# Optimization experiments

Measured on AMD Instinct MI355X. Metric: run time of the kernel, lower is better.

## Reference

```python
import jax, jax.numpy as jnp
import numpy as np

D_MODEL = 1024
H = 16
D_K = D_MODEL // H
NEG = -1e9


def setup_inputs() -> dict:
    key = jax.random.key(0)
    ks = jax.random.split(key, 13)
    B, S = 4, 2048
    q = jax.random.normal(ks[0], (B, S, D_MODEL), dtype=jnp.float32)
    k = jax.random.normal(ks[1], (B, S, D_MODEL), dtype=jnp.float32)
    v = jax.random.normal(ks[2], (B, S, D_MODEL), dtype=jnp.float32)
    mask = jax.random.randint(ks[3], (B, 1, S, S), 0, 2, dtype=jnp.int32)
    s = 1.0 / np.sqrt(D_MODEL)
    wq = jax.random.uniform(ks[4], (D_MODEL, D_MODEL), jnp.float32, -s, s)
    bq = jax.random.uniform(ks[5], (D_MODEL,), jnp.float32, -s, s)
    wk = jax.random.uniform(ks[6], (D_MODEL, D_MODEL), jnp.float32, -s, s)
    bk = jax.random.uniform(ks[7], (D_MODEL,), jnp.float32, -s, s)
    wv = jax.random.uniform(ks[8], (D_MODEL, D_MODEL), jnp.float32, -s, s)
    bv = jax.random.uniform(ks[9], (D_MODEL,), jnp.float32, -s, s)
    wo = jax.random.uniform(ks[10], (D_MODEL, D_MODEL), jnp.float32, -s, s)
    bo = jax.random.uniform(ks[11], (D_MODEL,), jnp.float32, -s, s)
    return {"q": q, "k": k, "v": v, "mask": mask,
            "wq": wq, "bq": bq, "wk": wk, "bk": bk,
            "wv": wv, "bv": bv, "wo": wo, "bo": bo}


def reference(q, k, v, mask, wq, bq, wk, bk, wv, bv, wo, bo):
    B, S, _ = q.shape
    # projections (torch Linear: x @ W.T + b)
    query = q @ wq.T + bq
    key_ = k @ wk.T + bk
    value = v @ wv.T + bv
    # [B, S, H, D_K] -> [B, H, S, D_K]
    query = query.reshape(B, S, H, D_K).transpose(0, 2, 1, 3)
    key_ = key_.reshape(B, S, H, D_K).transpose(0, 2, 1, 3)
    value = value.reshape(B, S, H, D_K).transpose(0, 2, 1, 3)
    scores = jnp.einsum('bhqd,bhkd->bhqk', query, key_) / jnp.sqrt(jnp.float32(D_K))
    scores = jnp.where(mask == 0, jnp.float32(NEG), scores)
    attn = jax.nn.softmax(scores, axis=-1)  # dropout p=0 -> identity
    x = jnp.einsum('bhqk,bhkd->bhqd', attn, value)
    x = x.transpose(0, 2, 1, 3).reshape(B, S, D_MODEL)
    return x @ wo.T + bo
```

## Files before the change

kernel.cpp:

```cpp
#include <hip/hip_runtime.h>
#include <stdint.h>
#include <stddef.h>


typedef unsigned short ushort_t;
typedef unsigned long long u64;
typedef __attribute__((ext_vector_type(8))) short short8;
typedef __attribute__((ext_vector_type(4))) float floatx4;
typedef __attribute__((ext_vector_type(4))) unsigned short ushort4v;
typedef __attribute__((ext_vector_type(4))) unsigned int uint4v;

#define QSCALE (0.125f * 1.4426950408889634f)

__device__ __forceinline__ ushort_t f2bf(float f) {
    union { float ff; unsigned int i; } v; v.ff = f;
    unsigned int u = v.i;
    return (ushort_t)((u + 0x7fffu + ((u >> 16) & 1u)) >> 16);
}
__device__ __forceinline__ unsigned int pk2(float a, float b) {
    unsigned int r;
    asm("v_cvt_pk_bf16_f32 %0, %1, %2" : "=v"(r) : "v"(a), "v"(b));
    return r;
}
__device__ __forceinline__ float fexp2(float x) {
#if __has_builtin(__builtin_amdgcn_exp2f)
    return __builtin_amdgcn_exp2f(x);
#else
    return exp2f(x);
#endif
}
__device__ __forceinline__ void g2l16(const void* g, void* l) {
    __builtin_amdgcn_global_load_lds(
        (const __attribute__((address_space(1))) void*)(uintptr_t)g,
        (__attribute__((address_space(3))) void*)(uint32_t)(uintptr_t)l,
        16, 0, 0);
}

__global__ __launch_bounds__(256) void conv_w4(
    const float* __restrict__ w0, const float* __restrict__ w1,
    const float* __restrict__ w2, const float* __restrict__ w3,
    ushort_t* __restrict__ out)
{
    const int seg = blockIdx.y;
    const float* src = (seg == 0) ? w0 : (seg == 1) ? w1 : (seg == 2) ? w2 : w3;
    const int i = blockIdx.x * 256 + threadIdx.x;
    const float4 v = ((const float4*)src)[i];
    ushort4v o;
    o.x = f2bf(v.x); o.y = f2bf(v.y); o.z = f2bf(v.z); o.w = f2bf(v.w);
    ((ushort4v*)(out + (size_t)seg * 1024 * 1024))[i] = o;
}

__global__ __launch_bounds__(256) void mask_pack(
    const int* __restrict__ m, u64* __restrict__ out)
{
    const int gid = blockIdx.x * 256 + threadIdx.x;
    const u64 bits = __ballot(m[gid] != 0);
    if ((threadIdx.x & 63) == 0) out[gid >> 6] = bits;
}

template <int AF32>
__device__ __forceinline__ void gemm_core(
    const void* __restrict__ Ain, const ushort_t* __restrict__ W,
    const float* __restrict__ bias, void* __restrict__ Cout,
    float scale, int mode)
{
    constexpr int N = 1024, K = 1024;
    __shared__ alignas(16) ushort_t As[2][128 * 32];
    __shared__ alignas(16) ushort_t Bs[2][128 * 32];

    const int tid  = threadIdx.x;
    const int lane = tid & 63;
    const int w    = tid >> 6;
    const int quad = lane >> 4;
    const int l16  = lane & 15;
    const int wm = w >> 1, wn = w & 1;
    const int bm = blockIdx.x * 128, bn = blockIdx.y * 128;

    const int ar0 = tid >> 2,         acs0 = ((tid & 3) ^ (ar0 & 3)) * 8;
    const int ar1 = (tid + 256) >> 2, acs1 = ((tid & 3) ^ (ar1 & 3)) * 8;

    const ushort_t* Wst0 = W + (size_t)(bn + ar0) * K + acs0;
    const ushort_t* Wst1 = W + (size_t)(bn + ar1) * K + acs1;

    const int arow = tid >> 1, ahalf = tid & 1;
    const float* Af = (const float*)Ain + (size_t)(bm + arow) * K + ahalf * 16;
    const int ac0 = ((2 * ahalf + 0) ^ (arow & 3)) * 8;
    const int ac1 = ((2 * ahalf + 1) ^ (arow & 3)) * 8;

    const ushort_t* Ast0 = (const ushort_t*)Ain + (size_t)(bm + ar0) * K + acs0;
    const ushort_t* Ast1 = (const ushort_t*)Ain + (size_t)(bm + ar1) * K + acs1;

    const int ksw = (quad ^ (l16 & 3)) * 8;
    int asoff[4], bsoff[4];
#pragma unroll
    for (int i = 0; i < 4; i++) {
        asoff[i] = (wm * 64 + i * 16 + l16) * 32 + ksw;
        bsoff[i] = (wn * 64 + i * 16 + l16) * 32 + ksw;
    }

    floatx4 acc[4][4] = {};

    if (AF32) {
        const float4* ap = (const float4*)Af;
        const float4 f0 = ap[0], f1 = ap[1], f2 = ap[2], f3 = ap[3];
        uint4v c0, c1;
        c0.x = pk2(f0.x, f0.y); c0.y = pk2(f0.z, f0.w);
        c0.z = pk2(f1.x, f1.y); c0.w = pk2(f1.z, f1.w);
        c1.x = pk2(f2.x, f2.y); c1.y = pk2(f2.z, f2.w);
        c1.z = pk2(f3.x, f3.y); c1.w = pk2(f3.z, f3.w);
        *(uint4v*)&As[0][arow * 32 + ac0] = c0;
        *(uint4v*)&As[0][arow * 32 + ac1] = c1;
    } else {
        g2l16(Ast0, &As[0][tid * 8]);
        g2l16(Ast1, &As[0][(tid + 256) * 8]);
    }
    g2l16(Wst0, &Bs[0][tid * 8]);
    g2l16(Wst1, &Bs[0][(tid + 256) * 8]);
    __syncthreads();

    int cur = 0;
    for (int kt = 0; kt < K; kt += 32) {
        const int nxt = kt + 32;
        float4 f0, f1, f2, f3;
        if (nxt < K) {
            if (AF32) {
                const float4* ap = (const float4*)(Af + nxt);
                f0 = ap[0]; f1 = ap[1]; f2 = ap[2]; f3 = ap[3];
            } else {
                g2l16(Ast0 + nxt, &As[cur ^ 1][tid * 8]);
                g2l16(Ast1 + nxt, &As[cur ^ 1][(tid + 256) * 8]);
            }
            g2l16(Wst0 + nxt, &Bs[cur ^ 1][tid * 8]);
            g2l16(Wst1 + nxt, &Bs[cur ^ 1][(tid + 256) * 8]);
        }

        short8 af[4], bf[4];
#pragma unroll
        for (int i = 0; i < 4; i++) af[i] = *(const short8*)&As[cur][asoff[i]];
#pragma unroll
        for (int i = 0; i < 4; i++) bf[i] = *(const short8*)&Bs[cur][bsoff[i]];
#pragma unroll
        for (int mi = 0; mi < 4; mi++)
#pragma unroll
            for (int ni = 0; ni < 4; ni++)
                acc[mi][ni] = __builtin_amdgcn_mfma_f32_16x16x32_bf16(
                    af[mi], bf[ni], acc[mi][ni], 0, 0, 0);

        if (AF32 && nxt < K) {
            uint4v c0, c1;
            c0.x = pk2(f0.x, f0.y); c0.y = pk2(f0.z, f0.w);
            c0.z = pk2(f1.x, f1.y); c0.w = pk2(f1.z, f1.w);
            c1.x = pk2(f2.x, f2.y); c1.y = pk2(f2.z, f2.w);
            c1.z = pk2(f3.x, f3.y); c1.w = pk2(f3.z, f3.w);
            *(uint4v*)&As[cur ^ 1][arow * 32 + ac0] = c0;
            *(uint4v*)&As[cur ^ 1][arow * 32 + ac1] = c1;
        }
        __syncthreads();
        cur ^= 1;
    }

#pragma unroll
    for (int ni = 0; ni < 4; ni++) {
        const int n = bn + wn * 64 + ni * 16 + l16;
        const float bv_ = bias[n];
#pragma unroll
        for (int mi = 0; mi < 4; mi++) {
            const int mbase = bm + wm * 64 + mi * 16 + quad * 4;
            if (mode == 2) {
                const int b_ = mbase >> 11, s0 = mbase & 2047;
                const int h = n >> 6, d = n & 63;
                ushort4v pk_;
#pragma unroll
                for (int r = 0; r < 4; r++)
                    pk_[r] = f2bf((acc[mi][ni][r] + bv_) * scale);
                *(ushort4v*)&((ushort_t*)Cout)[
                    (((size_t)(b_ * 16 + h)) * 64 + d) * 2048 + s0] = pk_;
            } else {
#pragma unroll
                for (int r = 0; r < 4; r++) {
                    const int m = mbase + r;
                    const float of = (acc[mi][ni][r] + bv_) * scale;
                    if (mode == 0) {
                        ((float*)Cout)[(size_t)m * N + n] = of;
                    } else {
                        const int b_ = m >> 11, s = m & 2047;
                        const int h = n >> 6, d = n & 63;
                        ((ushort_t*)Cout)[(((size_t)(b_ * 16 + h)) * 2048 + s) * 64 + d]
                            = f2bf(of);
                    }
                }
            }
        }
    }
}

__global__ __launch_bounds__(256, 2) void gemm_qkv(
    const float* __restrict__ q, const float* __restrict__ k,
    const float* __restrict__ v, const ushort_t* __restrict__ Wb,
    const float* __restrict__ bq, const float* __restrict__ bk,
    const float* __restrict__ bv,
    ushort_t* __restrict__ Qp, ushort_t* __restrict__ Kp,
    ushort_t* __restrict__ Vtp)
{
    const int z = blockIdx.z;
    const float* A = (z == 0) ? q : (z == 1) ? k : v;
    const ushort_t* W = Wb + (size_t)z * 1024 * 1024;
    const float* bi = (z == 0) ? bq : (z == 1) ? bk : bv;
    void* C = (z == 0) ? (void*)Qp : (z == 1) ? (void*)Kp : (void*)Vtp;
    const float sc = (z == 0) ? QSCALE : 1.0f;
    const int mode = (z == 2) ? 2 : 1;
    gemm_core<1>(A, W, bi, C, sc, mode);
}

__global__ __launch_bounds__(256, 2) void gemm_out(
    const ushort_t* __restrict__ X, const ushort_t* __restrict__ W,
    const float* __restrict__ bo, float* __restrict__ out)
{
    gemm_core<0>(X, W, bo, out, 1.0f, 0);
}

__global__ __launch_bounds__(256, 4) void attn(
    const ushort_t* __restrict__ Q,
    const ushort_t* __restrict__ Kk,
    const ushort_t* __restrict__ Vt,
    const u64* __restrict__ mb,
    ushort_t* __restrict__ X)
{
    constexpr int S = 2048;
    __shared__ alignas(16) ushort_t Ks[2][64 * 64];
    __shared__ alignas(16) ushort_t Vs[2][64 * 64];
    __shared__ alignas(16) ushort_t Ps[4][16 * 64];

    const int tid  = threadIdx.x;
    const int lane = tid & 63;
    const int w    = tid >> 6;
    const int quad = lane >> 4;
    const int l16  = lane & 15;
    const int bh = blockIdx.x;
    const int b  = bh >> 4, h = bh & 15;
    const int qbase = blockIdx.y * 64 + w * 16;
    const int qlane = qbase + l16;

    const int r0 = tid >> 3,         cs0 = ((tid & 7) ^ (r0 & 7)) * 8;
    const int r1 = (tid + 256) >> 3, cs1 = ((tid & 7) ^ (r1 & 7)) * 8;

    const ushort_t* Kst0 = &Kk[((size_t)bh * S + r0) * 64 + cs0];
    const ushort_t* Kst1 = &Kk[((size_t)bh * S + r1) * 64 + cs1];
    const ushort_t* Vst0 = &Vt[((size_t)bh * 64 + r0) * S + cs0];
    const ushort_t* Vst1 = &Vt[((size_t)bh * 64 + r1) * S + cs1];

    const int swz = l16 & 7;
    int kvoff[2][4], pfoff[2], pwoff[4];
#pragma unroll
    for (int ks = 0; ks < 2; ks++) {
        pfoff[ks] = l16 * 64 + (((ks * 4 + quad) ^ swz) * 8);
#pragma unroll
        for (int ni = 0; ni < 4; ni++)
            kvoff[ks][ni] = (ni * 16 + l16) * 64 + (((ks * 4 + quad) ^ swz) * 8);
    }
#pragma unroll
    for (int ni = 0; ni < 4; ni++)
        pwoff[ni] = l16 * 64 + (((ni * 2 + (quad >> 1)) ^ swz) * 8) + (quad & 1) * 4;
    ushort_t* Psw = &Ps[w][0];

    short8 qf[2];
#pragma unroll
    for (int ks = 0; ks < 2; ks++)
        qf[ks] = *(const short8*)&Q[((size_t)bh * S + qlane) * 64 + ks * 32 + quad * 8];

    short8 onesv;
#pragma unroll
    for (int i = 0; i < 8; i++) onesv[i] = (short)0x3F80;

    const u64* mrow = mb + ((size_t)b * S + qlane) * 32;

    floatx4 o[4] = {};
    floatx4 lf = {};

    g2l16(Kst0, &Ks[0][tid * 8]);
    g2l16(Kst1, &Ks[0][(tid + 256) * 8]);
    g2l16(Vst0, &Vs[0][tid * 8]);
    g2l16(Vst1, &Vs[0][(tid + 256) * 8]);
    __syncthreads();

    int cur = 0;
    for (int kt = 0; kt < 32; kt++) {
        if (kt < 31) {
            g2l16(Kst0 + (kt + 1) * 4096, &Ks[cur ^ 1][tid * 8]);
            g2l16(Kst1 + (kt + 1) * 4096, &Ks[cur ^ 1][(tid + 256) * 8]);
            g2l16(Vst0 + (kt + 1) * 64,   &Vs[cur ^ 1][tid * 8]);
            g2l16(Vst1 + (kt + 1) * 64,   &Vs[cur ^ 1][(tid + 256) * 8]);
        }
        const ushort_t* Ksc = &Ks[cur][0];
        const ushort_t* Vsc = &Vs[cur][0];

        floatx4 s[4] = {};
#pragma unroll
        for (int ks = 0; ks < 2; ks++)
#pragma unroll
            for (int ni = 0; ni < 4; ni++)
                s[ni] = __builtin_amdgcn_mfma_f32_16x16x32_bf16(
                    *(const short8*)&Ksc[kvoff[ks][ni]], qf[ks], s[ni], 0, 0, 0);

        const u64 mw = mrow[kt];
#pragma unroll
        for (int ni = 0; ni < 4; ni++) {
            const unsigned int t = (unsigned int)(mw >> (ni * 16 + quad * 4));
#pragma unroll
            for (int r = 0; r < 4; r++)
                s[ni][r] = (t & (1u << r)) ? fexp2(s[ni][r]) : 0.f;
        }

#pragma unroll
        for (int ni = 0; ni < 4; ni++) {
            const unsigned int lo = pk2(s[ni][0], s[ni][1]);
            const unsigned int hi = pk2(s[ni][2], s[ni][3]);
            const unsigned long long dv = ((unsigned long long)hi << 32) | lo;
            *(unsigned long long*)&Psw[pwoff[ni]] = dv;
        }

#pragma unroll
        for (int ks = 0; ks < 2; ks++) {
            const short8 pf = *(const short8*)&Psw[pfoff[ks]];
            lf = __builtin_amdgcn_mfma_f32_16x16x32_bf16(onesv, pf, lf, 0, 0, 0);
#pragma unroll
            for (int ni = 0; ni < 4; ni++)
                o[ni] = __builtin_amdgcn_mfma_f32_16x16x32_bf16(
                    *(const short8*)&Vsc[kvoff[ks][ni]], pf, o[ni], 0, 0, 0);
        }
        __syncthreads();
        cur ^= 1;
    }

    const float inv = 1.0f / lf[0];
#pragma unroll
    for (int ni = 0; ni < 4; ni++) {
        ushort4v pk_;
#pragma unroll
        for (int r = 0; r < 4; r++) pk_[r] = f2bf(o[ni][r] * inv);
        *(ushort4v*)&X[((size_t)b * S + qlane) * 1024 + h * 64 + ni * 16 + quad * 4] = pk_;
    }
}

extern "C" void kernel_launch(void* const* d_in, const int* in_sizes, int n_in,
                              void* d_out, int out_size, void* d_ws, size_t ws_size,
                              hipStream_t stream) {
    const float* q    = (const float*)d_in[0];
    const float* k    = (const float*)d_in[1];
    const float* v    = (const float*)d_in[2];
    const int*   mask = (const int*)d_in[3];
    const float* wq   = (const float*)d_in[4];
    const float* bq   = (const float*)d_in[5];
    const float* wk   = (const float*)d_in[6];
    const float* bk   = (const float*)d_in[7];
    const float* wv   = (const float*)d_in[8];
    const float* bv   = (const float*)d_in[9];
    const float* wo   = (const float*)d_in[10];
    const float* bo   = (const float*)d_in[11];

    const size_t MB = 1024 * 1024;
    uint8_t* ws = (uint8_t*)d_ws;
    ushort_t* Wb   = (ushort_t*)(ws);
    u64*      mbits= (u64*)(ws + 8 * MB);
    ushort_t* Qp   = (ushort_t*)(ws + 10 * MB);
    ushort_t* Kp   = (ushort_t*)(ws + 26 * MB);
    ushort_t* Vtp  = (ushort_t*)(ws + 42 * MB);
    ushort_t* Xp   = (ushort_t*)(ws + 58 * MB);

    dim3 blk(256);
    const int gW = (1024 * 1024) / 1024;
    const int gM = (4 * 2048 * 2048) / 256;

    conv_w4<<<dim3(gW, 4), blk, 0, stream>>>(wq, wk, wv, wo, Wb);
    mask_pack<<<gM, blk, 0, stream>>>(mask, mbits);

    gemm_qkv<<<dim3(64, 8, 3), blk, 0, stream>>>(q, k, v, Wb, bq, bk, bv,
                                                 Qp, Kp, Vtp);

    attn<<<dim3(64, 32), blk, 0, stream>>>(Qp, Kp, Vtp, mbits, Xp);

    gemm_out<<<dim3(64, 8), blk, 0, stream>>>(Xp, Wb + 3 * MB, bo, (float*)d_out);
}
```

Before: 430.8 us.

## Pre-convert activations to bf16 and triple-buffer GEMM with async loads

Adds a separate kernel that converts the fp32 q/k/v activations to bf16 so the QKV GEMM can load its A tiles with direct global-to-LDS copies instead of register loads plus in-loop conversion. The GEMM main loop becomes a three-stage LDS ring with explicit vmcnt waits and a single barrier per k-step, keeping two tiles in flight. The launch-bounds occupancy hint rises from 2 to 3 blocks. The trade is an extra pass over the activations in memory (read fp32, write bf16) and more LDS per block. Xp and Qb share a workspace region, which is safe only because the QKV GEMM finishes before attention writes Xp.

After: 419.5 us. 1.03x faster.

```diff
diff --git a/kernel.cpp b/kernel.cpp
--- a/kernel.cpp
+++ b/kernel.cpp
@@ -50,6 +50,24 @@
     ((ushort4v*)(out + (size_t)seg * 1024 * 1024))[i] = o;
 }
 
+__global__ __launch_bounds__(256) void cvt_a(
+    const float* __restrict__ q, const float* __restrict__ k,
+    const float* __restrict__ v,
+    ushort_t* __restrict__ Qb, ushort_t* __restrict__ Kb,
+    ushort_t* __restrict__ Vb)
+{
+    const int z = blockIdx.y;
+    const float* src = (z == 0) ? q : (z == 1) ? k : v;
+    ushort_t* dst = (z == 0) ? Qb : (z == 1) ? Kb : Vb;
+    const int i = blockIdx.x * 256 + threadIdx.x;
+    const float4 f0 = ((const float4*)src)[i * 2];
+    const float4 f1 = ((const float4*)src)[i * 2 + 1];
+    uint4v c;
+    c.x = pk2(f0.x, f0.y); c.y = pk2(f0.z, f0.w);
+    c.z = pk2(f1.x, f1.y); c.w = pk2(f1.z, f1.w);
+    ((uint4v*)dst)[i] = c;
+}
+
 __global__ __launch_bounds__(256) void mask_pack(
     const int* __restrict__ m, u64* __restrict__ out)
 {
@@ -58,15 +76,14 @@
     if ((threadIdx.x & 63) == 0) out[gid >> 6] = bits;
 }
 
-template <int AF32>
 __device__ __forceinline__ void gemm_core(
-    const void* __restrict__ Ain, const ushort_t* __restrict__ W,
+    const ushort_t* __restrict__ Ain, const ushort_t* __restrict__ W,
     const float* __restrict__ bias, void* __restrict__ Cout,
     float scale, int mode)
 {
     constexpr int N = 1024, K = 1024;
-    __shared__ alignas(16) ushort_t As[2][128 * 32];
-    __shared__ alignas(16) ushort_t Bs[2][128 * 32];
+    __shared__ alignas(16) ushort_t As[3][128 * 32];
+    __shared__ alignas(16) ushort_t Bs[3][128 * 32];
 
     const int tid  = threadIdx.x;
     const int lane = tid & 63;
@@ -78,17 +95,10 @@
 
     const int ar0 = tid >> 2,         acs0 = ((tid & 3) ^ (ar0 & 3)) * 8;
     const int ar1 = (tid + 256) >> 2, acs1 = ((tid & 3) ^ (ar1 & 3)) * 8;
-
+    const ushort_t* Ast0 = Ain + (size_t)(bm + ar0) * K + acs0;
+    const ushort_t* Ast1 = Ain + (size_t)(bm + ar1) * K + acs1;
     const ushort_t* Wst0 = W + (size_t)(bn + ar0) * K + acs0;
     const ushort_t* Wst1 = W + (size_t)(bn + ar1) * K + acs1;
-
-    const int arow = tid >> 1, ahalf = tid & 1;
-    const float* Af = (const float*)Ain + (size_t)(bm + arow) * K + ahalf * 16;
-    const int ac0 = ((2 * ahalf + 0) ^ (arow & 3)) * 8;
-    const int ac1 = ((2 * ahalf + 1) ^ (arow & 3)) * 8;
-
-    const ushort_t* Ast0 = (const ushort_t*)Ain + (size_t)(bm + ar0) * K + acs0;
-    const ushort_t* Ast1 = (const ushort_t*)Ain + (size_t)(bm + ar1) * K + acs1;
 
     const int ksw = (quad ^ (l16 & 3)) * 8;
     int asoff[4], bsoff[4];
@@ -100,64 +110,51 @@
 
     floatx4 acc[4][4] = {};
 
-    if (AF32) {
-        const float4* ap = (const float4*)Af;
-        const float4 f0 = ap[0], f1 = ap[1], f2 = ap[2], f3 = ap[3];
-        uint4v c0, c1;
-        c0.x = pk2(f0.x, f0.y); c0.y = pk2(f0.z, f0.w);
-        c0.z = pk2(f1.x, f1.y); c0.w = pk2(f1.z, f1.w);
-        c1.x = pk2(f2.x, f2.y); c1.y = pk2(f2.z, f2.w);
-        c1.z = pk2(f3.x, f3.y); c1.w = pk2(f3.z, f3.w);
-        *(uint4v*)&As[0][arow * 32 + ac0] = c0;
-        *(uint4v*)&As[0][arow * 32 + ac1] = c1;
-    } else {
-        g2l16(Ast0, &As[0][tid * 8]);
-        g2l16(Ast1, &As[0][(tid + 256) * 8]);
-    }
-    g2l16(Wst0, &Bs[0][tid * 8]);
-    g2l16(Wst1, &Bs[0][(tid + 256) * 8]);
-    __syncthreads();
-
-    int cur = 0;
-    for (int kt = 0; kt < K; kt += 32) {
-        const int nxt = kt + 32;
-        float4 f0, f1, f2, f3;
-        if (nxt < K) {
-            if (AF32) {
-                const float4* ap = (const float4*)(Af + nxt);
-                f0 = ap[0]; f1 = ap[1]; f2 = ap[2]; f3 = ap[3];
-            } else {
-                g2l16(Ast0 + nxt, &As[cur ^ 1][tid * 8]);
-                g2l16(Ast1 + nxt, &As[cur ^ 1][(tid + 256) * 8]);
-            }
-            g2l16(Wst0 + nxt, &Bs[cur ^ 1][tid * 8]);
-            g2l16(Wst1 + nxt, &Bs[cur ^ 1][(tid + 256) * 8]);
-        }
-
-        short8 af[4], bf[4];
-#pragma unroll
-        for (int i = 0; i < 4; i++) af[i] = *(const short8*)&As[cur][asoff[i]];
-#pragma unroll
-        for (int i = 0; i < 4; i++) bf[i] = *(const short8*)&Bs[cur][bsoff[i]];
-#pragma unroll
-        for (int mi = 0; mi < 4; mi++)
-#pragma unroll
-            for (int ni = 0; ni < 4; ni++)
-                acc[mi][ni] = __builtin_amdgcn_mfma_f32_16x16x32_bf16(
-                    af[mi], bf[ni], acc[mi][ni], 0, 0, 0);
-
-        if (AF32 && nxt < K) {
-            uint4v c0, c1;
-            c0.x = pk2(f0.x, f0.y); c0.y = pk2(f0.z, f0.w);
-            c0.z = pk2(f1.x, f1.y); c0.w = pk2(f1.z, f1.w);
-            c1.x = pk2(f2.x, f2.y); c1.y = pk2(f2.z, f2.w);
-            c1.z = pk2(f3.x, f3.y); c1.w = pk2(f3.z, f3.w);
-            *(uint4v*)&As[cur ^ 1][arow * 32 + ac0] = c0;
-            *(uint4v*)&As[cur ^ 1][arow * 32 + ac1] = c1;
-        }
-        __syncthreads();
-        cur ^= 1;
-    }
+    g2l16(Ast0,      &As[0][tid * 8]);
+    g2l16(Ast1,      &As[0][(tid + 256) * 8]);
+    g2l16(Wst0,      &Bs[0][tid * 8]);
+    g2l16(Wst1,      &Bs[0][(tid + 256) * 8]);
+    g2l16(Ast0 + 32, &As[1][tid * 8]);
+    g2l16(Ast1 + 32, &As[1][(tid + 256) * 8]);
+    g2l16(Wst0 + 32, &Bs[1][tid * 8]);
+    g2l16(Wst1 + 32, &Bs[1][(tid + 256) * 8]);
+
+#define GITER(SLOT, NSLOT, KOFF, DO_ISSUE, TOPW) do {                         \
+    asm volatile("s_waitcnt " TOPW);                                          \
+    asm volatile("s_waitcnt lgkmcnt(0)");                                     \
+    __builtin_amdgcn_sched_barrier(0);                                        \
+    __builtin_amdgcn_s_barrier();                                             \
+    __builtin_amdgcn_sched_barrier(0);                                        \
+    if (DO_ISSUE) {                                                           \
+        g2l16(Ast0 + (KOFF), &As[NSLOT][tid * 8]);                            \
+        g2l16(Ast1 + (KOFF), &As[NSLOT][(tid + 256) * 8]);                    \
+        g2l16(Wst0 + (KOFF), &Bs[NSLOT][tid * 8]);                            \
+        g2l16(Wst1 + (KOFF), &Bs[NSLOT][(tid + 256) * 8]);                    \
+    }                                                                         \
+    {                                                                         \
+        short8 af[4], bf[4];                                                  \
+        _Pragma("unroll")                                                     \
+        for (int i = 0; i < 4; i++) af[i] = *(const short8*)&As[SLOT][asoff[i]];\
+        _Pragma("unroll")                                                     \
+        for (int i = 0; i < 4; i++) bf[i] = *(const short8*)&Bs[SLOT][bsoff[i]];\
+        _Pragma("unroll")                                                     \
+        for (int mi = 0; mi < 4; mi++)                                        \
+        _Pragma("unroll")                                                     \
+        for (int ni = 0; ni < 4; ni++)                                        \
+            acc[mi][ni] = __builtin_amdgcn_mfma_f32_16x16x32_bf16(            \
+                af[mi], bf[ni], acc[mi][ni], 0, 0, 0);                        \
+    }                                                                         \
+} while (0)
+
+    for (int j = 0; j < 10; ++j) {
+        const int kt = j * 96;
+        GITER(0, 2, kt + 64,  true, "vmcnt(4)");
+        GITER(1, 0, kt + 96,  true, "vmcnt(4)");
+        GITER(2, 1, kt + 128, true, "vmcnt(4)");
+    }
+    GITER(0, 0, 0, false, "vmcnt(4)");
+    GITER(1, 0, 0, false, "vmcnt(0)");
+#undef GITER
 
 #pragma unroll
     for (int ni = 0; ni < 4; ni++) {
@@ -194,29 +191,29 @@
     }
 }
 
-__global__ __launch_bounds__(256, 2) void gemm_qkv(
-    const float* __restrict__ q, const float* __restrict__ k,
-    const float* __restrict__ v, const ushort_t* __restrict__ Wb,
+__global__ __launch_bounds__(256, 3) void gemm_qkv(
+    const ushort_t* __restrict__ Qb, const ushort_t* __restrict__ Kb,
+    const ushort_t* __restrict__ Vb, const ushort_t* __restrict__ Wb,
     const float* __restrict__ bq, const float* __restrict__ bk,
     const float* __restrict__ bv,
     ushort_t* __restrict__ Qp, ushort_t* __restrict__ Kp,
     ushort_t* __restrict__ Vtp)
 {
     const int z = blockIdx.z;
-    const float* A = (z == 0) ? q : (z == 1) ? k : v;
+    const ushort_t* A = (z == 0) ? Qb : (z == 1) ? Kb : Vb;
     const ushort_t* W = Wb + (size_t)z * 1024 * 1024;
     const float* bi = (z == 0) ? bq : (z == 1) ? bk : bv;
     void* C = (z == 0) ? (void*)Qp : (z == 1) ? (void*)Kp : (void*)Vtp;
     const float sc = (z == 0) ? QSCALE : 1.0f;
     const int mode = (z == 2) ? 2 : 1;
-    gemm_core<1>(A, W, bi, C, sc, mode);
-}
-
-__global__ __launch_bounds__(256, 2) void gemm_out(
+    gemm_core(A, W, bi, C, sc, mode);
+}
+
+__global__ __launch_bounds__(256, 3) void gemm_out(
     const ushort_t* __restrict__ X, const ushort_t* __restrict__ W,
     const float* __restrict__ bo, float* __restrict__ out)
 {
-    gemm_core<0>(X, W, bo, out, 1.0f, 0);
+    gemm_core(X, W, bo, out, 1.0f, 0);
 }
 
 __global__ __launch_bounds__(256, 4) void attn(
@@ -366,6 +363,9 @@
     ushort_t* Kp   = (ushort_t*)(ws + 26 * MB);
     ushort_t* Vtp  = (ushort_t*)(ws + 42 * MB);
     ushort_t* Xp   = (ushort_t*)(ws + 58 * MB);
+    ushort_t* Qb   = (ushort_t*)(ws + 58 * MB);
+    ushort_t* Kb   = (ushort_t*)(ws + 74 * MB);
+    ushort_t* Vb   = (ushort_t*)(ws + 90 * MB);
 
     dim3 blk(256);
     const int gW = (1024 * 1024) / 1024;
@@ -373,8 +373,9 @@
 
     conv_w4<<<dim3(gW, 4), blk, 0, stream>>>(wq, wk, wv, wo, Wb);
     mask_pack<<<gM, blk, 0, stream>>>(mask, mbits);
-
-    gemm_qkv<<<dim3(64, 8, 3), blk, 0, stream>>>(q, k, v, Wb, bq, bk, bv,
+    cvt_a<<<dim3(4096, 3), blk, 0, stream>>>(q, k, v, Qb, Kb, Vb);
+
+    gemm_qkv<<<dim3(64, 8, 3), blk, 0, stream>>>(Qb, Kb, Vb, Wb, bq, bk, bv,
                                                  Qp, Kp, Vtp);
 
     attn<<<dim3(64, 32), blk, 0, stream>>>(Qp, Kp, Vtp, mbits, Xp);
```
